# Kernel optimization log

Hardware: AMD Instinct MI355X
Metric: run time of the kernel (lower is better)

Reference implementation:

```python
import jax, jax.numpy as jnp
import numpy as np

N = 50000
E = 800000
NEG_SLOPE = 0.2


def setup_inputs() -> dict:
    key = jax.random.key(0)
    ks = jax.random.split(key, 12)
    feat = jax.random.normal(ks[0], (N, 256), dtype=jnp.float32)
    src = jax.random.randint(ks[1], (E,), 0, N, dtype=jnp.int32)
    dst = jax.random.randint(ks[2], (E,), 0, N, dtype=jnp.int32)
    # layer 1: in=256 -> H=4, D=64 (concat 256)
    W1 = jax.random.normal(ks[3], (256, 256), dtype=jnp.float32) * (1.0 / np.sqrt(256))
    attn_l1 = jax.random.normal(ks[4], (4, 64), dtype=jnp.float32) * 0.1
    attn_r1 = jax.random.normal(ks[5], (4, 64), dtype=jnp.float32) * 0.1
    bias1 = jnp.zeros((256,), dtype=jnp.float32)
    # layer 2: in=256 -> H=1, D=128
    W2 = jax.random.normal(ks[6], (256, 128), dtype=jnp.float32) * (1.0 / np.sqrt(256))
    attn_l2 = jax.random.normal(ks[7], (1, 128), dtype=jnp.float32) * 0.1
    attn_r2 = jax.random.normal(ks[8], (1, 128), dtype=jnp.float32) * 0.1
    bias2 = jnp.zeros((128,), dtype=jnp.float32)
    return {"feat": feat, "src": src, "dst": dst,
            "W1": W1, "attn_l1": attn_l1, "attn_r1": attn_r1, "bias1": bias1,
            "W2": W2, "attn_l2": attn_l2, "attn_r2": attn_r2, "bias2": bias2}


def gat_conv(feat, src, dst, W, attn_l, attn_r, bias, apply_relu):
    H, D = attn_l.shape
    n = feat.shape[0]
    ft = (feat @ W).reshape(n, H, D)                      # [N,H,D]
    el = jnp.einsum('nhd,hd->nh', ft, attn_l)             # [N,H]
    er = jnp.einsum('nhd,hd->nh', ft, attn_r)             # [N,H]
    e = el[src] + er[dst]                                 # [E,H]  u_add_v
    e = jnp.where(e > 0, e, NEG_SLOPE * e)                # leaky_relu
    # edge softmax grouped by dst
    m = jax.ops.segment_max(e, dst, num_segments=n)       # [N,H]
    ex = jnp.exp(e - m[dst])
    denom = jax.ops.segment_sum(ex, dst, num_segments=n)  # [N,H]
    a = ex / denom[dst]                                   # [E,H]
    msg = ft[src] * a[:, :, None]                         # [E,H,D]
    out = jax.ops.segment_sum(msg, dst, num_segments=n)   # [N,H,D]
    out = out + bias.reshape(1, H, D)
    out = out.reshape(n, H * D)                           # concat_out
    if apply_relu:
        out = jax.nn.relu(out)
    return out


def reference(feat, src, dst, W1, attn_l1, attn_r1, bias1, W2, attn_l2, attn_r2, bias2):
    h = gat_conv(feat, src, dst, W1, attn_l1, attn_r1, bias1, apply_relu=True)
    h = gat_conv(h, src, dst, W2, attn_l2, attn_r2, bias2, apply_relu=False)
    return h
```

## Files before the change

### kernel.cpp

```cpp
#include <hip/hip_runtime.h>
#include <hip/hip_bf16.h>

#define NEG_SLOPE 0.2f

typedef short s16x8 __attribute__((ext_vector_type(8)));
typedef float f32x4 __attribute__((ext_vector_type(4)));

__device__ __forceinline__ unsigned short f2bf(float f) {
    unsigned int u = __float_as_uint(f);
    unsigned int r = (u + 0x7fffu + ((u >> 16) & 1u)) >> 16;
    return (unsigned short)r;
}
__device__ __forceinline__ float bf2f(unsigned int us) {
    return __uint_as_float(us << 16);
}


__global__ void count_wl_k(const int* __restrict__ dst, int* __restrict__ counts, int E,
                           const float* __restrict__ W1, const float* __restrict__ al1,
                           const float* __restrict__ ar1,
                           const float* __restrict__ W2, const float* __restrict__ al2,
                           const float* __restrict__ ar2,
                           float* __restrict__ wl1, float* __restrict__ wl2) {
    if (blockIdx.x == 0) {
        int k = threadIdx.x;
        #pragma unroll
        for (int h = 0; h < 4; h++) {
            float sl = 0.f, sr = 0.f;
            #pragma unroll 8
            for (int d = 0; d < 64; d++) {
                float wv = W1[k * 256 + h * 64 + d];
                sl = fmaf(wv, al1[h * 64 + d], sl);
                sr = fmaf(wv, ar1[h * 64 + d], sr);
            }
            wl1[k * 8 + h] = sl;
            wl1[k * 8 + 4 + h] = sr;
        }
        float sl = 0.f, sr = 0.f;
        #pragma unroll 8
        for (int d = 0; d < 128; d++) {
            float wv = W2[k * 128 + d];
            sl = fmaf(wv, al2[d], sl);
            sr = fmaf(wv, ar2[d], sr);
        }
        wl2[k * 2 + 0] = sl;
        wl2[k * 2 + 1] = sr;
        return;
    }
    int e = (blockIdx.x - 1) * 256 + threadIdx.x;
    if (e < E) atomicAdd(&counts[dst[e]], 1);
}


__global__ __launch_bounds__(1024) void scan_k(const int* __restrict__ counts,
                                               int* __restrict__ flags,
                                               int* __restrict__ offsets,
                                               int* __restrict__ cursor, int n) {
    __shared__ int s_wt[16];
    __shared__ int s_base;
    const int tid = threadIdx.x, lane = tid & 63, wid = tid >> 6;
    const int bid = blockIdx.x;
    const int i = bid * 1024 + tid;
    int v = (i < n) ? counts[i] : 0;
    int incl = v;
    #pragma unroll
    for (int o = 1; o < 64; o <<= 1) {
        int t = __shfl_up(incl, o);
        if (lane >= o) incl += t;
    }
    if (lane == 63) s_wt[wid] = incl;
    __syncthreads();
    if (tid == 0) {
        int r = 0;
        #pragma unroll
        for (int w = 0; w < 16; w++) { int t = s_wt[w]; s_wt[w] = r; r += t; }
        atomicExch(&flags[bid], r + 1);
        s_base = 0;
    }
    __syncthreads();
    if (wid == 0) {
        int contrib = 0;
        if (lane < bid) {
            int f;
            while ((f = atomicAdd(&flags[lane], 0)) == 0) {}
            contrib = f - 1;
        }
        #pragma unroll
        for (int o = 32; o > 0; o >>= 1) contrib += __shfl_xor(contrib, o);
        if (lane == 0) s_base = contrib;
    }
    __syncthreads();
    if (i < n) {
        int excl = s_base + s_wt[wid] + (incl - v);
        offsets[i + 1] = excl + v;
        cursor[i] = excl;
    }
    if (bid == 0 && tid == 0) offsets[0] = 0;
}

__global__ void fill_csr_k(const int* __restrict__ src, const int* __restrict__ dst,
                           int* __restrict__ cursor, int* __restrict__ csr_src, int E) {
    int e = blockIdx.x * blockDim.x + threadIdx.x;
    if (e < E) {
        int pos = atomicAdd(&cursor[dst[e]], 1);
        csr_src[pos] = src[e];
    }
}


template <int MODE>
__global__ __launch_bounds__(256) void gemm_k(const float* __restrict__ A,
                                              const float* __restrict__ B,
                                              unsigned short* __restrict__ Cb,
                                              int M, int K, int Nc,
                                              const float* __restrict__ wl,
                                              float* __restrict__ el,
                                              float* __restrict__ er) {
    __shared__ __align__(16) unsigned short As_hi[128][40], As_lo[128][40];
    __shared__ __align__(16) unsigned short Bs_hi[64][40],  Bs_lo[64][40];
    __shared__ float s_wla[256], s_wlb[256];
    __shared__ float s_red[128][2];

    const int tid = threadIdx.x;
    const int lane = tid & 63, wid = tid >> 6;
    const int by = blockIdx.x;
    const int row0 = blockIdx.y * 128;
    const int col0 = by * 64;
    const int wm = (wid & 1) * 64;
    const int wn = (wid >> 1) * 32;
    const int quad = lane >> 4, mrow = lane & 15;

    const int a_r = tid >> 1;
    const int a_k = (tid & 1) * 16;
    const int b_k = tid >> 3;
    const int b_n = (tid & 7) * 8;
    const bool a_valid = (row0 + a_r) < M;

    if (MODE == 1) { s_wla[tid] = wl[tid * 8 + by]; s_wlb[tid] = wl[tid * 8 + 4 + by]; }
    else           { s_wla[tid] = wl[tid * 2 + by]; }
    __syncthreads();

    f32x4 acc[4][2];
    #pragma unroll
    for (int i = 0; i < 4; i++)
        #pragma unroll
        for (int j = 0; j < 2; j++) acc[i][j] = f32x4{0.f, 0.f, 0.f, 0.f};
    float pa = 0.f, pb = 0.f;

    for (int k0 = 0; k0 < K; k0 += 32) {
        float af[16];
        if (a_valid) {
            const float* ap = &A[(size_t)(row0 + a_r) * K + k0 + a_k];
            #pragma unroll
            for (int q = 0; q < 4; q++) {
                float4 t = *(const float4*)(ap + q * 4);
                af[q * 4 + 0] = t.x; af[q * 4 + 1] = t.y;
                af[q * 4 + 2] = t.z; af[q * 4 + 3] = t.w;
            }
        } else {
            #pragma unroll
            for (int q = 0; q < 16; q++) af[q] = 0.f;
        }
        #pragma unroll
        for (int p = 0; p < 16; p++) {
            pa = fmaf(af[p], s_wla[k0 + a_k + p], pa);
            if (MODE == 1) pb = fmaf(af[p], s_wlb[k0 + a_k + p], pb);
        }
        unsigned int* dh = (unsigned int*)&As_hi[a_r][a_k];
        unsigned int* dl = (unsigned int*)&As_lo[a_r][a_k];
        #pragma unroll
        for (int p = 0; p < 8; p++) {
            unsigned short h0 = f2bf(af[2 * p]), h1 = f2bf(af[2 * p + 1]);
            unsigned short l0 = f2bf(af[2 * p] - bf2f(h0));
            unsigned short l1 = f2bf(af[2 * p + 1] - bf2f(h1));
            dh[p] = (unsigned int)h0 | ((unsigned int)h1 << 16);
            dl[p] = (unsigned int)l0 | ((unsigned int)l1 << 16);
        }
        {
            const float* bp = &B[(size_t)(k0 + b_k) * Nc + col0 + b_n];
            float4 t0 = *(const float4*)(bp);
            float4 t1 = *(const float4*)(bp + 4);
            float bf[8] = {t0.x, t0.y, t0.z, t0.w, t1.x, t1.y, t1.z, t1.w};
            #pragma unroll
            for (int x = 0; x < 8; x++) {
                unsigned short h = f2bf(bf[x]);
                unsigned short l = f2bf(bf[x] - bf2f(h));
                Bs_hi[b_n + x][b_k] = h;
                Bs_lo[b_n + x][b_k] = l;
            }
        }
        __syncthreads();

        s16x8 ah[4], al4[4], bh[2], bl[2];
        #pragma unroll
        for (int i = 0; i < 4; i++) {
            ah[i]  = *(const s16x8*)&As_hi[wm + 16 * i + mrow][quad * 8];
            al4[i] = *(const s16x8*)&As_lo[wm + 16 * i + mrow][quad * 8];
        }
        #pragma unroll
        for (int j = 0; j < 2; j++) {
            bh[j] = *(const s16x8*)&Bs_hi[wn + 16 * j + mrow][quad * 8];
            bl[j] = *(const s16x8*)&Bs_lo[wn + 16 * j + mrow][quad * 8];
        }
        #pragma unroll
        for (int i = 0; i < 4; i++)
            #pragma unroll
            for (int j = 0; j < 2; j++) {
                acc[i][j] = __builtin_amdgcn_mfma_f32_16x16x32_bf16(ah[i],  bh[j], acc[i][j], 0, 0, 0);
                acc[i][j] = __builtin_amdgcn_mfma_f32_16x16x32_bf16(ah[i],  bl[j], acc[i][j], 0, 0, 0);
                acc[i][j] = __builtin_amdgcn_mfma_f32_16x16x32_bf16(al4[i], bh[j], acc[i][j], 0, 0, 0);
            }
        __syncthreads();
    }

    if (a_k == 16) { s_red[a_r][0] = pa; if (MODE == 1) s_red[a_r][1] = pb; }
    __syncthreads();
    if (a_k == 0 && a_valid) {
        float ra = pa + s_red[a_r][0];
        if (MODE == 1) {
            float rb = pb + s_red[a_r][1];
            el[(row0 + a_r) * 4 + by] = ra;
            er[(row0 + a_r) * 4 + by] = rb;
        } else {
            (by == 0 ? el : er)[row0 + a_r] = ra;
        }
    }

    #pragma unroll
    for (int i = 0; i < 4; i++) {
        #pragma unroll
        for (int j = 0; j < 2; j++) {
            int col = col0 + wn + 16 * j + mrow;
            int rbase = row0 + wm + 16 * i + quad * 4;
            #pragma unroll
            for (int r = 0; r < 4; r++) {
                int row = rbase + r;
                if (row < M) Cb[(size_t)row * Nc + col] = f2bf(acc[i][j][r]);
            }
        }
    }
}


__device__ __forceinline__ void fma8(float* acc, float wgt, uint4 u) {
    acc[0] = fmaf(wgt, bf2f(u.x & 0xffff), acc[0]);
    acc[1] = fmaf(wgt, bf2f(u.x >> 16),    acc[1]);
    acc[2] = fmaf(wgt, bf2f(u.y & 0xffff), acc[2]);
    acc[3] = fmaf(wgt, bf2f(u.y >> 16),    acc[3]);
    acc[4] = fmaf(wgt, bf2f(u.z & 0xffff), acc[4]);
    acc[5] = fmaf(wgt, bf2f(u.z >> 16),    acc[5]);
    acc[6] = fmaf(wgt, bf2f(u.w & 0xffff), acc[6]);
    acc[7] = fmaf(wgt, bf2f(u.w >> 16),    acc[7]);
}

template <int H, int D, bool RELU>
__global__ __launch_bounds__(256) void fagg_k(const unsigned short* __restrict__ ft,
                                              const float* __restrict__ el,
                                              const float* __restrict__ er,
                                              const int* __restrict__ offsets,
                                              const int* __restrict__ csr_src,
                                              const float* __restrict__ bias,
                                              float* __restrict__ out, int n_nodes) {
    constexpr int HD = H * D;
    constexpr int LPE = HD / 8;
    constexpr int EPI = 64 / LPE;
    const int lane = threadIdx.x & 63;
    const int w = threadIdx.x >> 6;
    const int n = blockIdx.x * 4 + w;
    __shared__ int   s_src[4][64];
    __shared__ float s_a[4][64 * H];
    if (n >= n_nodes) return;
    const int off = offsets[n];
    const int deg = offsets[n + 1] - off;
    const int lane_sub = lane & (LPE - 1);
    const int q = lane / LPE;
    const int c0 = lane_sub * 8;
    const int h_of = c0 / D;

    float ern[H];
    #pragma unroll
    for (int h = 0; h < H; h++) ern[h] = er[n * H + h];

    float acc[8];
    #pragma unroll
    for (int t = 0; t < 8; t++) acc[t] = 0.f;

    const int* s_src_w = s_src[w];
    const float* s_a_w = s_a[w];
    const uint4* fp = ((const uint4*)ft) + lane_sub;

    if (deg <= 64) {
        const bool act = lane < deg;
        int sv = act ? csr_src[off + lane] : 0;
        s_src[w][lane] = sv;
        float evr[H];
        if constexpr (H == 4) {
            float4 e4 = ((const float4*)el)[sv];
            evr[0] = e4.x; evr[1] = e4.y; evr[2] = e4.z; evr[3] = e4.w;
        } else {
            evr[0] = el[sv];
        }
        int p0, p1, p2, p3;
        {
            p0 = s_src_w[q]; p1 = s_src_w[EPI + q];
            p2 = s_src_w[2 * EPI + q]; p3 = s_src_w[3 * EPI + q];
        }
        uint4 u0 = fp[(size_t)p0 * LPE];
        uint4 u1 = fp[(size_t)p1 * LPE];
        uint4 u2 = fp[(size_t)p2 * LPE];
        uint4 u3 = fp[(size_t)p3 * LPE];
        float ev[H], m[H];
        #pragma unroll
        for (int h = 0; h < H; h++) {
            float t = evr[h] + ern[h];
            t = t > 0.f ? t : NEG_SLOPE * t;
            ev[h] = act ? t : -1e30f;
            m[h] = ev[h];
        }
        #pragma unroll
        for (int h = 0; h < H; h++)
            for (int o = 32; o > 0; o >>= 1) m[h] = fmaxf(m[h], __shfl_xor(m[h], o));
        float ex[H], sm[H];
        #pragma unroll
        for (int h = 0; h < H; h++) { ex[h] = act ? __expf(ev[h] - m[h]) : 0.f; sm[h] = ex[h]; }
        #pragma unroll
        for (int h = 0; h < H; h++)
            for (int o = 32; o > 0; o >>= 1) sm[h] += __shfl_xor(sm[h], o);
        #pragma unroll
        for (int h = 0; h < H; h++)
            s_a[w][lane * H + h] = ex[h] * (sm[h] > 0.f ? 1.f / sm[h] : 0.f);
        fma8(acc, s_a_w[(q) * H + h_of], u0);
        fma8(acc, s_a_w[(EPI + q) * H + h_of], u1);
        fma8(acc, s_a_w[(2 * EPI + q) * H + h_of], u2);
        fma8(acc, s_a_w[(3 * EPI + q) * H + h_of], u3);
        const int rc = (deg + EPI - 1) & ~(EPI - 1);
        int i = 4 * EPI;
        for (; i + 4 * EPI <= rc; i += 4 * EPI) {
            int e0 = i + q, e1 = i + EPI + q, e2 = i + 2 * EPI + q, e3 = i + 3 * EPI + q;
            int s0 = s_src_w[e0], s1 = s_src_w[e1], s2 = s_src_w[e2], s3 = s_src_w[e3];
            uint4 v0 = fp[(size_t)s0 * LPE];
            uint4 v1 = fp[(size_t)s1 * LPE];
            uint4 v2 = fp[(size_t)s2 * LPE];
            uint4 v3 = fp[(size_t)s3 * LPE];
            float w0 = s_a_w[e0 * H + h_of], w1 = s_a_w[e1 * H + h_of];
            float w2 = s_a_w[e2 * H + h_of], w3 = s_a_w[e3 * H + h_of];
            fma8(acc, w0, v0); fma8(acc, w1, v1); fma8(acc, w2, v2); fma8(acc, w3, v3);
        }
        for (; i < rc; i += EPI) {
            int e = i + q;
            int s = s_src_w[e];
            uint4 v = fp[(size_t)s * LPE];
            fma8(acc, s_a_w[e * H + h_of], v);
        }
    } else {
        float m[H];
        #pragma unroll
        for (int h = 0; h < H; h++) m[h] = -1e30f;
        for (int i = lane; i < deg; i += 64) {
            int sv = csr_src[off + i];
            if constexpr (H == 4) {
                float4 e4 = ((const float4*)el)[sv];
                float tmp[4] = {e4.x, e4.y, e4.z, e4.w};
                #pragma unroll
                for (int h = 0; h < 4; h++) {
                    float t = tmp[h] + ern[h];
                    t = t > 0.f ? t : NEG_SLOPE * t;
                    m[h] = fmaxf(m[h], t);
                }
            } else {
                float t = el[sv] + ern[0];
                t = t > 0.f ? t : NEG_SLOPE * t;
                m[0] = fmaxf(m[0], t);
            }
        }
        #pragma unroll
        for (int h = 0; h < H; h++)
            for (int o = 32; o > 0; o >>= 1) m[h] = fmaxf(m[h], __shfl_xor(m[h], o));
        float sm[H];
        #pragma unroll
        for (int h = 0; h < H; h++) sm[h] = 0.f;
        for (int i = lane; i < deg; i += 64) {
            int sv = csr_src[off + i];
            if constexpr (H == 4) {
                float4 e4 = ((const float4*)el)[sv];
                float tmp[4] = {e4.x, e4.y, e4.z, e4.w};
                #pragma unroll
                for (int h = 0; h < 4; h++) {
                    float t = tmp[h] + ern[h];
                    t = t > 0.f ? t : NEG_SLOPE * t;
                    sm[h] += __expf(t - m[h]);
                }
            } else {
                float t = el[sv] + ern[0];
                t = t > 0.f ? t : NEG_SLOPE * t;
                sm[0] += __expf(t - m[0]);
            }
        }
        #pragma unroll
        for (int h = 0; h < H; h++)
            for (int o = 32; o > 0; o >>= 1) sm[h] += __shfl_xor(sm[h], o);
        float inv[H];
        #pragma unroll
        for (int h = 0; h < H; h++) inv[h] = (sm[h] > 0.f) ? (1.f / sm[h]) : 0.f;
        for (int base = 0; base < deg; base += 64) {
            const bool act2 = base + lane < deg;
            int sv = act2 ? csr_src[off + base + lane] : 0;
            s_src[w][lane] = sv;
            float exh[H];
            if constexpr (H == 4) {
                float4 e4 = ((const float4*)el)[sv];
                float tmp[4] = {e4.x, e4.y, e4.z, e4.w};
                #pragma unroll
                for (int h = 0; h < 4; h++) {
                    float t = tmp[h] + ern[h];
                    t = t > 0.f ? t : NEG_SLOPE * t;
                    exh[h] = act2 ? __expf(t - m[h]) * inv[h] : 0.f;
                }
            } else {
                float t = el[sv] + ern[0];
                t = t > 0.f ? t : NEG_SLOPE * t;
                exh[0] = act2 ? __expf(t - m[0]) * inv[0] : 0.f;
            }
            #pragma unroll
            for (int h = 0; h < H; h++) s_a[w][lane * H + h] = exh[h];
            int cnt = min(64, deg - base);
            int rc = (cnt + EPI - 1) & ~(EPI - 1);
            int i = 0;
            for (; i + 4 * EPI <= rc; i += 4 * EPI) {
                int e0 = i + q, e1 = i + EPI + q, e2 = i + 2 * EPI + q, e3 = i + 3 * EPI + q;
                int s0 = s_src_w[e0], s1 = s_src_w[e1], s2 = s_src_w[e2], s3 = s_src_w[e3];
                uint4 v0 = fp[(size_t)s0 * LPE];
                uint4 v1 = fp[(size_t)s1 * LPE];
                uint4 v2 = fp[(size_t)s2 * LPE];
                uint4 v3 = fp[(size_t)s3 * LPE];
                float w0 = s_a_w[e0 * H + h_of], w1 = s_a_w[e1 * H + h_of];
                float w2 = s_a_w[e2 * H + h_of], w3 = s_a_w[e3 * H + h_of];
                fma8(acc, w0, v0); fma8(acc, w1, v1); fma8(acc, w2, v2); fma8(acc, w3, v3);
            }
            for (; i < rc; i += EPI) {
                int e = i + q;
                int s = s_src_w[e];
                uint4 v = fp[(size_t)s * LPE];
                fma8(acc, s_a_w[e * H + h_of], v);
            }
        }
    }

    #pragma unroll
    for (int t = 0; t < 8; t++) {
        #pragma unroll
        for (int s = LPE; s < 64; s <<= 1) acc[t] += __shfl_xor(acc[t], s);
    }
    if (lane < LPE) {
        float4 b0 = ((const float4*)bias)[lane * 2];
        float4 b1 = ((const float4*)bias)[lane * 2 + 1];
        float4 o0{acc[0] + b0.x, acc[1] + b0.y, acc[2] + b0.z, acc[3] + b0.w};
        float4 o1{acc[4] + b1.x, acc[5] + b1.y, acc[6] + b1.z, acc[7] + b1.w};
        if (RELU) {
            o0.x = fmaxf(o0.x, 0.f); o0.y = fmaxf(o0.y, 0.f);
            o0.z = fmaxf(o0.z, 0.f); o0.w = fmaxf(o0.w, 0.f);
            o1.x = fmaxf(o1.x, 0.f); o1.y = fmaxf(o1.y, 0.f);
            o1.z = fmaxf(o1.z, 0.f); o1.w = fmaxf(o1.w, 0.f);
        }
        float4* op = (float4*)out + (size_t)n * (HD / 4) + lane * 2;
        op[0] = o0;
        op[1] = o1;
    }
}


extern "C" void kernel_launch(void* const* d_in, const int* in_sizes, int n_in,
                              void* d_out, int out_size, void* d_ws, size_t ws_size,
                              hipStream_t stream) {
    const float* feat    = (const float*)d_in[0];
    const int*   src     = (const int*)d_in[1];
    const int*   dst     = (const int*)d_in[2];
    const float* W1      = (const float*)d_in[3];
    const float* attn_l1 = (const float*)d_in[4];
    const float* attn_r1 = (const float*)d_in[5];
    const float* bias1   = (const float*)d_in[6];
    const float* W2      = (const float*)d_in[7];
    const float* attn_l2 = (const float*)d_in[8];
    const float* attn_r2 = (const float*)d_in[9];
    const float* bias2   = (const float*)d_in[10];
    float* out = (float*)d_out;

    const int N = in_sizes[0] / 256;
    const int E = in_sizes[1];
    const int NB = (N + 1023) / 1024;

    char* ws = (char*)d_ws;
    size_t o = 0;
    auto alloc = [&](size_t bytes) -> void* {
        void* p = ws + o;
        o = (o + bytes + 255) & ~(size_t)255;
        return p;
    };
    int* counts  = (int*)alloc((size_t)(N + 64) * 4);
    int* flags   = counts + N;
    int* cursor  = (int*)alloc((size_t)N * 4);
    int* offsets = (int*)alloc((size_t)(N + 1) * 4);
    int* csr_src = (int*)alloc((size_t)E * 4);
    float* wl1 = (float*)alloc(256 * 8 * 4);
    float* wl2 = (float*)alloc(256 * 2 * 4);
    float* el1 = (float*)alloc((size_t)N * 4 * 4);
    float* er1 = (float*)alloc((size_t)N * 4 * 4);
    float* el2 = (float*)alloc((size_t)N * 4);
    float* er2 = (float*)alloc((size_t)N * 4);
    unsigned short* ft1b = (unsigned short*)alloc((size_t)N * 256 * 2);
    float* h1 = (float*)alloc((size_t)N * 256 * 4);
    unsigned short* ft2b = ft1b;

    hipMemsetAsync(counts, 0, (size_t)(N + 64) * 4, stream);
    count_wl_k<<<1 + (E + 255) / 256, 256, 0, stream>>>(dst, counts, E,
        W1, attn_l1, attn_r1, W2, attn_l2, attn_r2, wl1, wl2);
    scan_k<<<NB, 1024, 0, stream>>>(counts, flags, offsets, cursor, N);
    fill_csr_k<<<(E + 255) / 256, 256, 0, stream>>>(src, dst, cursor, csr_src, E);

    gemm_k<1><<<dim3(4, (N + 127) / 128), 256, 0, stream>>>(feat, W1, ft1b, N, 256, 256,
                                                            wl1, el1, er1);
    fagg_k<4, 64, true><<<(N + 3) / 4, 256, 0, stream>>>(ft1b, el1, er1, offsets, csr_src,
                                                         bias1, h1, N);

    gemm_k<2><<<dim3(2, (N + 127) / 128), 256, 0, stream>>>(h1, W2, ft2b, N, 256, 128,
                                                            wl2, el2, er2);
    fagg_k<1, 128, false><<<(N + 3) / 4, 256, 0, stream>>>(ft2b, el2, er2, offsets, csr_src,
                                                           bias2, out, N);
}
```

Before: 388.1 us.

## Pre-split operands to bf16 hi/lo, fuse layer-2 prep into aggregation epilogue

After: 415.7 us. 7.1% more time.

```diff
diff --git a/kernel.cpp b/kernel.cpp
--- a/kernel.cpp
+++ b/kernel.cpp
@@ -21,9 +21,14 @@
                            const float* __restrict__ ar1,
                            const float* __restrict__ W2, const float* __restrict__ al2,
                            const float* __restrict__ ar2,
-                           float* __restrict__ wl1, float* __restrict__ wl2) {
-    if (blockIdx.x == 0) {
-        int k = threadIdx.x;
+                           float* __restrict__ wl1, float* __restrict__ wl2l,
+                           float* __restrict__ wl2r,
+                           unsigned int* __restrict__ wt1h, unsigned int* __restrict__ wt1l,
+                           unsigned int* __restrict__ wt2h, unsigned int* __restrict__ wt2l) {
+    const int bid = blockIdx.x;
+    const int tid = threadIdx.x;
+    if (bid == 0) {
+        int k = tid;
         #pragma unroll
         for (int h = 0; h < 4; h++) {
             float sl = 0.f, sr = 0.f;
@@ -43,11 +48,35 @@
             sl = fmaf(wv, al2[d], sl);
             sr = fmaf(wv, ar2[d], sr);
         }
-        wl2[k * 2 + 0] = sl;
-        wl2[k * 2 + 1] = sr;
+        wl2l[k] = sl;
+        wl2r[k] = sr;
         return;
     }
-    int e = (blockIdx.x - 1) * 256 + threadIdx.x;
+    if (bid == 1) {
+        int n = tid;
+        for (int k = 0; k < 256; k += 2) {
+            float v0 = W1[k * 256 + n], v1 = W1[(k + 1) * 256 + n];
+            unsigned short h0 = f2bf(v0), h1 = f2bf(v1);
+            unsigned short l0 = f2bf(v0 - bf2f(h0)), l1 = f2bf(v1 - bf2f(h1));
+            wt1h[n * 128 + k / 2] = (unsigned int)h0 | ((unsigned int)h1 << 16);
+            wt1l[n * 128 + k / 2] = (unsigned int)l0 | ((unsigned int)l1 << 16);
+        }
+        return;
+    }
+    if (bid == 2) {
+        int n = tid;
+        if (n < 128) {
+            for (int k = 0; k < 256; k += 2) {
+                float v0 = W2[k * 128 + n], v1 = W2[(k + 1) * 128 + n];
+                unsigned short h0 = f2bf(v0), h1 = f2bf(v1);
+                unsigned short l0 = f2bf(v0 - bf2f(h0)), l1 = f2bf(v1 - bf2f(h1));
+                wt2h[n * 128 + k / 2] = (unsigned int)h0 | ((unsigned int)h1 << 16);
+                wt2l[n * 128 + k / 2] = (unsigned int)l0 | ((unsigned int)l1 << 16);
+            }
+        }
+        return;
+    }
+    int e = (bid - 3) * 256 + tid;
     if (e < E) atomicAdd(&counts[dst[e]], 1);
 }
 
@@ -108,18 +137,71 @@
 }
 
 
-template <int MODE>
-__global__ __launch_bounds__(256) void gemm_k(const float* __restrict__ A,
-                                              const float* __restrict__ B,
+__global__ __launch_bounds__(256) void split1_k(const float* __restrict__ feat,
+                                                const float* __restrict__ wl1,
+                                                unsigned short* __restrict__ Ahi,
+                                                unsigned short* __restrict__ Alo,
+                                                float* __restrict__ el,
+                                                float* __restrict__ er, int N) {
+    __shared__ float s_wl[2048];
+    const int tid = threadIdx.x;
+    #pragma unroll
+    for (int j = 0; j < 8; j++) s_wl[tid * 8 + j] = wl1[tid * 8 + j];
+    __syncthreads();
+    const int r = tid >> 5, c = tid & 31;
+    const int row = blockIdx.x * 8 + r;
+    if (row >= N) return;
+    const int c0 = c * 8;
+    float4 f0 = *(const float4*)&feat[(size_t)row * 256 + c0];
+    float4 f1 = *(const float4*)&feat[(size_t)row * 256 + c0 + 4];
+    float v[8] = {f0.x, f0.y, f0.z, f0.w, f1.x, f1.y, f1.z, f1.w};
+    float pa[4] = {0.f, 0.f, 0.f, 0.f}, pb[4] = {0.f, 0.f, 0.f, 0.f};
+    #pragma unroll
+    for (int j = 0; j < 8; j++) {
+        const float* wv = &s_wl[(c0 + j) * 8];
+        #pragma unroll
+        for (int h = 0; h < 4; h++) {
+            pa[h] = fmaf(v[j], wv[h], pa[h]);
+            pb[h] = fmaf(v[j], wv[4 + h], pb[h]);
+        }
+    }
+    unsigned int hi[4], lo[4];
+    #pragma unroll
+    for (int j = 0; j < 4; j++) {
+        unsigned short h0 = f2bf(v[2 * j]), h1 = f2bf(v[2 * j + 1]);
+        unsigned short l0 = f2bf(v[2 * j] - bf2f(h0)), l1 = f2bf(v[2 * j + 1] - bf2f(h1));
+        hi[j] = (unsigned int)h0 | ((unsigned int)h1 << 16);
+        lo[j] = (unsigned int)l0 | ((unsigned int)l1 << 16);
+    }
+    *(uint4*)&Ahi[(size_t)row * 256 + c0] = uint4{hi[0], hi[1], hi[2], hi[3]};
+    *(uint4*)&Alo[(size_t)row * 256 + c0] = uint4{lo[0], lo[1], lo[2], lo[3]};
+    #pragma unroll
+    for (int o = 1; o <= 16; o <<= 1) {
+        #pragma unroll
+        for (int h = 0; h < 4; h++) {
+            pa[h] += __shfl_xor(pa[h], o);
+            pb[h] += __shfl_xor(pb[h], o);
+        }
+    }
+    if (c == 0) {
+        *(float4*)&el[(size_t)row * 4] = float4{pa[0], pa[1], pa[2], pa[3]};
+        *(float4*)&er[(size_t)row * 4] = float4{pb[0], pb[1], pb[2], pb[3]};
+    }
+}
+
+
+__device__ __forceinline__ int sw(int row, int chunk) {
+    return row * 32 + ((chunk ^ (row & 3)) * 8);
+}
+
+__global__ __launch_bounds__(256) void gemm_k(const unsigned short* __restrict__ Ahi,
+                                              const unsigned short* __restrict__ Alo,
+                                              const unsigned short* __restrict__ Bth,
+                                              const unsigned short* __restrict__ Btl,
                                               unsigned short* __restrict__ Cb,
-                                              int M, int K, int Nc,
-                                              const float* __restrict__ wl,
-                                              float* __restrict__ el,
-                                              float* __restrict__ er) {
-    __shared__ __align__(16) unsigned short As_hi[128][40], As_lo[128][40];
-    __shared__ __align__(16) unsigned short Bs_hi[64][40],  Bs_lo[64][40];
-    __shared__ float s_wla[256], s_wlb[256];
-    __shared__ float s_red[128][2];
+                                              int M, int Nc) {
+    __shared__ __align__(16) unsigned short As_hi[128 * 32], As_lo[128 * 32];
+    __shared__ __align__(16) unsigned short Bs_hi[64 * 32],  Bs_lo[64 * 32];
 
     const int tid = threadIdx.x;
     const int lane = tid & 63, wid = tid >> 6;
@@ -130,77 +212,53 @@
     const int wn = (wid >> 1) * 32;
     const int quad = lane >> 4, mrow = lane & 15;
 
-    const int a_r = tid >> 1;
-    const int a_k = (tid & 1) * 16;
-    const int b_k = tid >> 3;
-    const int b_n = (tid & 7) * 8;
-    const bool a_valid = (row0 + a_r) < M;
-
-    if (MODE == 1) { s_wla[tid] = wl[tid * 8 + by]; s_wlb[tid] = wl[tid * 8 + 4 + by]; }
-    else           { s_wla[tid] = wl[tid * 2 + by]; }
-    __syncthreads();
+    const int row_a = tid >> 1, ca = tid & 1;
+    const int row_b = tid >> 2, cb = tid & 3;
+    const size_t abase = (size_t)(row0 + row_a) * 256 + ca * 8;
+    const size_t bbase = (size_t)(col0 + row_b) * 256 + cb * 8;
 
     f32x4 acc[4][2];
     #pragma unroll
     for (int i = 0; i < 4; i++)
         #pragma unroll
         for (int j = 0; j < 2; j++) acc[i][j] = f32x4{0.f, 0.f, 0.f, 0.f};
-    float pa = 0.f, pb = 0.f;
-
-    for (int k0 = 0; k0 < K; k0 += 32) {
-        float af[16];
-        if (a_valid) {
-            const float* ap = &A[(size_t)(row0 + a_r) * K + k0 + a_k];
-            #pragma unroll
-            for (int q = 0; q < 4; q++) {
-                float4 t = *(const float4*)(ap + q * 4);
-                af[q * 4 + 0] = t.x; af[q * 4 + 1] = t.y;
-                af[q * 4 + 2] = t.z; af[q * 4 + 3] = t.w;
-            }
-        } else {
-            #pragma unroll
-            for (int q = 0; q < 16; q++) af[q] = 0.f;
-        }
-        #pragma unroll
-        for (int p = 0; p < 16; p++) {
-            pa = fmaf(af[p], s_wla[k0 + a_k + p], pa);
-            if (MODE == 1) pb = fmaf(af[p], s_wlb[k0 + a_k + p], pb);
-        }
-        unsigned int* dh = (unsigned int*)&As_hi[a_r][a_k];
-        unsigned int* dl = (unsigned int*)&As_lo[a_r][a_k];
-        #pragma unroll
-        for (int p = 0; p < 8; p++) {
-            unsigned short h0 = f2bf(af[2 * p]), h1 = f2bf(af[2 * p + 1]);
-            unsigned short l0 = f2bf(af[2 * p] - bf2f(h0));
-            unsigned short l1 = f2bf(af[2 * p + 1] - bf2f(h1));
-            dh[p] = (unsigned int)h0 | ((unsigned int)h1 << 16);
-            dl[p] = (unsigned int)l0 | ((unsigned int)l1 << 16);
-        }
-        {
-            const float* bp = &B[(size_t)(k0 + b_k) * Nc + col0 + b_n];
-            float4 t0 = *(const float4*)(bp);
-            float4 t1 = *(const float4*)(bp + 4);
-            float bf[8] = {t0.x, t0.y, t0.z, t0.w, t1.x, t1.y, t1.z, t1.w};
-            #pragma unroll
-            for (int x = 0; x < 8; x++) {
-                unsigned short h = f2bf(bf[x]);
-                unsigned short l = f2bf(bf[x] - bf2f(h));
-                Bs_hi[b_n + x][b_k] = h;
-                Bs_lo[b_n + x][b_k] = l;
-            }
-        }
+
+    uint4 rah0, rah1, ral0, ral1, rbh, rbl;
+    rah0 = *(const uint4*)&Ahi[abase];
+    rah1 = *(const uint4*)&Ahi[abase + 16];
+    ral0 = *(const uint4*)&Alo[abase];
+    ral1 = *(const uint4*)&Alo[abase + 16];
+    rbh  = *(const uint4*)&Bth[bbase];
+    rbl  = *(const uint4*)&Btl[bbase];
+
+    for (int k0 = 0; k0 < 256; k0 += 32) {
+        *(uint4*)&As_hi[sw(row_a, ca)]     = rah0;
+        *(uint4*)&As_hi[sw(row_a, ca + 2)] = rah1;
+        *(uint4*)&As_lo[sw(row_a, ca)]     = ral0;
+        *(uint4*)&As_lo[sw(row_a, ca + 2)] = ral1;
+        *(uint4*)&Bs_hi[sw(row_b, cb)]     = rbh;
+        *(uint4*)&Bs_lo[sw(row_b, cb)]     = rbl;
         __syncthreads();
-
+        if (k0 < 224) {
+            rah0 = *(const uint4*)&Ahi[abase + k0 + 32];
+            rah1 = *(const uint4*)&Ahi[abase + k0 + 48];
+            ral0 = *(const uint4*)&Alo[abase + k0 + 32];
+            ral1 = *(const uint4*)&Alo[abase + k0 + 48];
+            rbh  = *(const uint4*)&Bth[bbase + k0 + 32];
+            rbl  = *(const uint4*)&Btl[bbase + k0 + 32];
+        }
         s16x8 ah[4], al4[4], bh[2], bl[2];
         #pragma unroll
         for (int i = 0; i < 4; i++) {
-            ah[i]  = *(const s16x8*)&As_hi[wm + 16 * i + mrow][quad * 8];
-            al4[i] = *(const s16x8*)&As_lo[wm + 16 * i + mrow][quad * 8];
+            int r = wm + 16 * i + mrow;
+            ah[i]  = *(const s16x8*)&As_hi[sw(r, quad)];
+            al4[i] = *(const s16x8*)&As_lo[sw(r, quad)];
         }
         #pragma unroll
         for (int j = 0; j < 2; j++) {
-            bh[j] = *(const s16x8*)&Bs_hi[wn + 16 * j + mrow][quad * 8];
-            bl[j] = *(const s16x8*)&Bs_lo[wn + 16 * j + mrow][quad * 8];
+            int r = wn + 16 * j + mrow;
+            bh[j] = *(const s16x8*)&Bs_hi[sw(r, quad)];
+            bl[j] = *(const s16x8*)&Bs_lo[sw(r, quad)];
         }
         #pragma unroll
         for (int i = 0; i < 4; i++)
@@ -211,19 +269,6 @@
                 acc[i][j] = __builtin_amdgcn_mfma_f32_16x16x32_bf16(al4[i], bh[j], acc[i][j], 0, 0, 0);
             }
         __syncthreads();
-    }
-
-    if (a_k == 16) { s_red[a_r][0] = pa; if (MODE == 1) s_red[a_r][1] = pb; }
-    __syncthreads();
-    if (a_k == 0 && a_valid) {
-        float ra = pa + s_red[a_r][0];
-        if (MODE == 1) {
-            float rb = pb + s_red[a_r][1];
-            el[(row0 + a_r) * 4 + by] = ra;
-            er[(row0 + a_r) * 4 + by] = rb;
-        } else {
-            (by == 0 ? el : er)[row0 + a_r] = ra;
-        }
     }
 
     #pragma unroll
@@ -253,14 +298,20 @@
     acc[7] = fmaf(wgt, bf2f(u.w >> 16),    acc[7]);
 }
 
-template <int H, int D, bool RELU>
+template <int H, int D, bool RELU, bool WP>
 __global__ __launch_bounds__(256) void fagg_k(const unsigned short* __restrict__ ft,
                                               const float* __restrict__ el,
                                               const float* __restrict__ er,
                                               const int* __restrict__ offsets,
                                               const int* __restrict__ csr_src,
                                               const float* __restrict__ bias,
-                                              float* __restrict__ out, int n_nodes) {
+                                              float* __restrict__ out, int n_nodes,
+                                              const float* __restrict__ wl2l,
+                                              const float* __restrict__ wl2r,
+                                              unsigned short* __restrict__ phi,
+                                              unsigned short* __restrict__ plo,
+                                              float* __restrict__ el2,
+                                              float* __restrict__ er2) {
     constexpr int HD = H * D;
     constexpr int LPE = HD / 8;
     constexpr int EPI = 64 / LPE;
@@ -300,11 +351,8 @@
         } else {
             evr[0] = el[sv];
         }
-        int p0, p1, p2, p3;
-        {
-            p0 = s_src_w[q]; p1 = s_src_w[EPI + q];
-            p2 = s_src_w[2 * EPI + q]; p3 = s_src_w[3 * EPI + q];
-        }
+        int p0 = s_src_w[q], p1 = s_src_w[EPI + q];
+        int p2 = s_src_w[2 * EPI + q], p3 = s_src_w[3 * EPI + q];
         uint4 u0 = fp[(size_t)p0 * LPE];
         uint4 u1 = fp[(size_t)p1 * LPE];
         uint4 u2 = fp[(size_t)p2 * LPE];
@@ -451,20 +499,58 @@
         #pragma unroll
         for (int s = LPE; s < 64; s <<= 1) acc[t] += __shfl_xor(acc[t], s);
     }
-    if (lane < LPE) {
-        float4 b0 = ((const float4*)bias)[lane * 2];
-        float4 b1 = ((const float4*)bias)[lane * 2 + 1];
-        float4 o0{acc[0] + b0.x, acc[1] + b0.y, acc[2] + b0.z, acc[3] + b0.w};
-        float4 o1{acc[4] + b1.x, acc[5] + b1.y, acc[6] + b1.z, acc[7] + b1.w};
-        if (RELU) {
-            o0.x = fmaxf(o0.x, 0.f); o0.y = fmaxf(o0.y, 0.f);
-            o0.z = fmaxf(o0.z, 0.f); o0.w = fmaxf(o0.w, 0.f);
-            o1.x = fmaxf(o1.x, 0.f); o1.y = fmaxf(o1.y, 0.f);
-            o1.z = fmaxf(o1.z, 0.f); o1.w = fmaxf(o1.w, 0.f);
-        }
-        float4* op = (float4*)out + (size_t)n * (HD / 4) + lane * 2;
-        op[0] = o0;
-        op[1] = o1;
+
+    if constexpr (WP) {
+        const int ls = lane & 31;
+        float4 b0 = ((const float4*)bias)[ls * 2];
+        float4 b1 = ((const float4*)bias)[ls * 2 + 1];
+        float v[8] = {acc[0] + b0.x, acc[1] + b0.y, acc[2] + b0.z, acc[3] + b0.w,
+                      acc[4] + b1.x, acc[5] + b1.y, acc[6] + b1.z, acc[7] + b1.w};
+        #pragma unroll
+        for (int t = 0; t < 8; t++) v[t] = fmaxf(v[t], 0.f);
+        if (lane < 32) {
+            uint4 hp, lp;
+            unsigned short h0, h1;
+            h0 = f2bf(v[0]); h1 = f2bf(v[1]);
+            hp.x = (unsigned int)h0 | ((unsigned int)h1 << 16);
+            lp.x = (unsigned int)f2bf(v[0] - bf2f(h0)) | ((unsigned int)f2bf(v[1] - bf2f(h1)) << 16);
+            h0 = f2bf(v[2]); h1 = f2bf(v[3]);
+            hp.y = (unsigned int)h0 | ((unsigned int)h1 << 16);
+            lp.y = (unsigned int)f2bf(v[2] - bf2f(h0)) | ((unsigned int)f2bf(v[3] - bf2f(h1)) << 16);
+            h0 = f2bf(v[4]); h1 = f2bf(v[5]);
+            hp.z = (unsigned int)h0 | ((unsigned int)h1 << 16);
+            lp.z = (unsigned int)f2bf(v[4] - bf2f(h0)) | ((unsigned int)f2bf(v[5] - bf2f(h1)) << 16);
+            h0 = f2bf(v[6]); h1 = f2bf(v[7]);
+            hp.w = (unsigned int)h0 | ((unsigned int)h1 << 16);
+            lp.w = (unsigned int)f2bf(v[6] - bf2f(h0)) | ((unsigned int)f2bf(v[7] - bf2f(h1)) << 16);
+            ((uint4*)phi)[(size_t)n * 32 + ls] = hp;
+            ((uint4*)plo)[(size_t)n * 32 + ls] = lp;
+        }
+        float4 wa0 = ((const float4*)wl2l)[ls * 2], wa1 = ((const float4*)wl2l)[ls * 2 + 1];
+        float4 wb0 = ((const float4*)wl2r)[ls * 2], wb1 = ((const float4*)wl2r)[ls * 2 + 1];
+        float pe = v[0] * wa0.x + v[1] * wa0.y + v[2] * wa0.z + v[3] * wa0.w +
+                   v[4] * wa1.x + v[5] * wa1.y + v[6] * wa1.z + v[7] * wa1.w;
+        float pr = v[0] * wb0.x + v[1] * wb0.y + v[2] * wb0.z + v[3] * wb0.w +
+                   v[4] * wb1.x + v[5] * wb1.y + v[6] * wb1.z + v[7] * wb1.w;
+        #pragma unroll
+        for (int o = 1; o <= 16; o <<= 1) { pe += __shfl_xor(pe, o); pr += __shfl_xor(pr, o); }
+        if (lane == 0) { el2[n] = pe; er2[n] = pr; }
+    } else {
+        if (lane < LPE) {
+            float4 b0 = ((const float4*)bias)[lane * 2];
+            float4 b1 = ((const float4*)bias)[lane * 2 + 1];
+            float4 o0{acc[0] + b0.x, acc[1] + b0.y, acc[2] + b0.z, acc[3] + b0.w};
+            float4 o1{acc[4] + b1.x, acc[5] + b1.y, acc[6] + b1.z, acc[7] + b1.w};
+            if (RELU) {
+                o0.x = fmaxf(o0.x, 0.f); o0.y = fmaxf(o0.y, 0.f);
+                o0.z = fmaxf(o0.z, 0.f); o0.w = fmaxf(o0.w, 0.f);
+                o1.x = fmaxf(o1.x, 0.f); o1.y = fmaxf(o1.y, 0.f);
+                o1.z = fmaxf(o1.z, 0.f); o1.w = fmaxf(o1.w, 0.f);
+            }
+            float4* op = (float4*)out + (size_t)n * (HD / 4) + lane * 2;
+            op[0] = o0;
+            op[1] = o1;
+        }
     }
 }
 
@@ -501,29 +587,39 @@
     int* cursor  = (int*)alloc((size_t)N * 4);
     int* offsets = (int*)alloc((size_t)(N + 1) * 4);
     int* csr_src = (int*)alloc((size_t)E * 4);
-    float* wl1 = (float*)alloc(256 * 8 * 4);
-    float* wl2 = (float*)alloc(256 * 2 * 4);
+    unsigned short* A1hi = (unsigned short*)alloc((size_t)N * 256 * 2);
+    unsigned short* A1lo = (unsigned short*)alloc((size_t)N * 256 * 2);
+    unsigned short* h1hi = A1hi;
+    unsigned short* h1lo = A1lo;
+    unsigned short* ft1b = (unsigned short*)alloc((size_t)N * 256 * 2);
+    unsigned short* ft2b = ft1b;
+    unsigned int* wt1h = (unsigned int*)alloc(256 * 128 * 4);
+    unsigned int* wt1l = (unsigned int*)alloc(256 * 128 * 4);
+    unsigned int* wt2h = (unsigned int*)alloc(128 * 128 * 4);
+    unsigned int* wt2l = (unsigned int*)alloc(128 * 128 * 4);
+    float* wl1  = (float*)alloc(256 * 8 * 4);
+    float* wl2l = (float*)alloc(256 * 4);
+    float* wl2r = (float*)alloc(256 * 4);
     float* el1 = (float*)alloc((size_t)N * 4 * 4);
     float* er1 = (float*)alloc((size_t)N * 4 * 4);
     float* el2 = (float*)alloc((size_t)N * 4);
     float* er2 = (float*)alloc((size_t)N * 4);
-    unsigned short* ft1b = (unsigned short*)alloc((size_t)N * 256 * 2);
-    float* h1 = (float*)alloc((size_t)N * 256 * 4);
-    unsigned short* ft2b = ft1b;
 
     hipMemsetAsync(counts, 0, (size_t)(N + 64) * 4, stream);
-    count_wl_k<<<1 + (E + 255) / 256, 256, 0, stream>>>(dst, counts, E,
-        W1, attn_l1, attn_r1, W2, attn_l2, attn_r2, wl1, wl2);
+    count_wl_k<<<3 + (E + 255) / 256, 256, 0, stream>>>(dst, counts, E,
+        W1, attn_l1, attn_r1, W2, attn_l2, attn_r2,
+        wl1, wl2l, wl2r, wt1h, wt1l, wt2h, wt2l);
     scan_k<<<NB, 1024, 0, stream>>>(counts, flags, offsets, cursor, N);
     fill_csr_k<<<(E + 255) / 256, 256, 0, stream>>>(src, dst, cursor, csr_src, E);
-
-    gemm_k<1><<<dim3(4, (N + 127) / 128), 256, 0, stream>>>(feat, W1, ft1b, N, 256, 256,
-                                                            wl1, el1, er1);
-    fagg_k<4, 64, true><<<(N + 3) / 4, 256, 0, stream>>>(ft1b, el1, er1, offsets, csr_src,
-                                                         bias1, h1, N);
-
-    gemm_k<2><<<dim3(2, (N + 127) / 128), 256, 0, stream>>>(h1, W2, ft2b, N, 256, 128,
-                                                            wl2, el2, er2);
-    fagg_k<1, 128, false><<<(N + 3) / 4, 256, 0, stream>>>(ft2b, el2, er2, offsets, csr_src,
-                                                           bias2, out, N);
-}
+    split1_k<<<(N + 7) / 8, 256, 0, stream>>>(feat, wl1, A1hi, A1lo, el1, er1, N);
+
+    gemm_k<<<dim3(4, (N + 127) / 128), 256, 0, stream>>>(A1hi, A1lo,
+        (const unsigned short*)wt1h, (const unsigned short*)wt1l, ft1b, N, 256);
+    fagg_k<4, 64, true, true><<<(N + 3) / 4, 256, 0, stream>>>(ft1b, el1, er1, offsets,
+        csr_src, bias1, nullptr, N, wl2l, wl2r, h1hi, h1lo, el2, er2);
+
+    gemm_k<<<dim3(2, (N + 127) / 128), 256, 0, stream>>>(h1hi, h1lo,
+        (const unsigned short*)wt2h, (const unsigned short*)wt2l, ft2b, N, 128);
+    fagg_k<1, 128, false, false><<<(N + 3) / 4, 256, 0, stream>>>(ft2b, el2, er2, offsets,
+        csr_src, bias2, out, N, nullptr, nullptr, nullptr, nullptr, nullptr, nullptr);
+}
```
